# Kernel optimization log

Hardware: AMD Instinct MI355X
Metric: run time of the kernel (lower is better)

## Reference

```python
import jax, jax.numpy as jnp
import numpy as np

H = 8          # num_heads in nn.MultiheadAttention
TOP_K = 3
LN_EPS = 1e-5


def _layer_norm(x, gamma, beta):
    mu = x.mean(axis=-1, keepdims=True)
    var = ((x - mu) ** 2).mean(axis=-1, keepdims=True)
    return (x - mu) * jax.lax.rsqrt(var + LN_EPS) * gamma + beta


def setup_inputs() -> dict:
    key = jax.random.key(0)
    ks = jax.random.split(key, 12)
    B, T, D, N = 4, 4096, 1024, 64
    s = 0.02
    return {
        "current_frame": jax.random.normal(ks[0], (B, T, D), jnp.float32),
        "entity_memory": jax.random.normal(ks[1], (B, N, D), jnp.float32),
        "in_proj_w": jax.random.normal(ks[2], (3 * D, D), jnp.float32) * s,
        "in_proj_b": jax.random.normal(ks[3], (3 * D,), jnp.float32) * s,
        "out_proj_w": jax.random.normal(ks[4], (D, D), jnp.float32) * s,
        "out_proj_b": jax.random.normal(ks[5], (D,), jnp.float32) * s,
        "ln_gamma": jnp.ones((3, D), jnp.float32),
        "ln_beta": jnp.zeros((3, D), jnp.float32),
        "w1": jax.random.normal(ks[6], (3, 2 * D, D), jnp.float32) * s,
        "b1": jax.random.normal(ks[7], (3, 2 * D), jnp.float32) * s,
        "w2": jax.random.normal(ks[8], (3, D, 2 * D), jnp.float32) * s,
        "b2": jax.random.normal(ks[9], (3, D), jnp.float32) * s,
        "gate_w": jax.random.normal(ks[10], (D, 2 * D), jnp.float32) * s,
        "gate_b": jax.random.normal(ks[11], (D,), jnp.float32) * s,
    }


def reference(current_frame, entity_memory, in_proj_w, in_proj_b,
              out_proj_w, out_proj_b, ln_gamma, ln_beta, w1, b1, w2, b2,
              gate_w, gate_b):
    B, T, D = current_frame.shape
    N = entity_memory.shape[1]
    hd = D // H

    # --- nn.MultiheadAttention(q=frame, k=v=entity_memory), batch_first ---
    wq, wk, wv = in_proj_w[:D], in_proj_w[D:2 * D], in_proj_w[2 * D:]
    bq, bk, bv = in_proj_b[:D], in_proj_b[D:2 * D], in_proj_b[2 * D:]
    q = (current_frame @ wq.T + bq).reshape(B, T, H, hd).transpose(0, 2, 1, 3)
    k = (entity_memory @ wk.T + bk).reshape(B, N, H, hd).transpose(0, 2, 1, 3)
    v = (entity_memory @ wv.T + bv).reshape(B, N, H, hd).transpose(0, 2, 1, 3)
    scores = jnp.einsum('bhtd,bhnd->bhtn', q, k) / jnp.sqrt(jnp.float32(hd))
    attn = jax.nn.softmax(scores, axis=-1)                     # [B,H,T,N]
    ctx = jnp.einsum('bhtn,bhnd->bhtd', attn, v)
    ctx = ctx.transpose(0, 2, 1, 3).reshape(B, T, D)
    attended = ctx @ out_proj_w.T + out_proj_b
    attn_weights = attn.mean(axis=1)                           # avg over heads [B,T,N]

    # --- residual consistency MLP stack ---
    x = current_frame + attended
    for i in range(ln_gamma.shape[0]):
        h = _layer_norm(x, ln_gamma[i], ln_beta[i])
        h = jax.nn.gelu(h @ w1[i].T + b1[i], approximate=False)
        x = x + h @ w2[i].T + b2[i]

    # --- gated EMA entity-memory update ---
    frame_summary = current_frame.mean(axis=1, keepdims=True)   # [B,1,D]
    mem_summary = entity_memory.mean(axis=1, keepdims=True)     # [B,1,D]
    gate = jax.nn.sigmoid(
        jnp.concatenate([frame_summary, mem_summary], axis=-1) @ gate_w.T + gate_b)
    new_mem = gate * frame_summary + (1.0 - gate) * mem_summary  # [B,1,D]

    top_k = min(TOP_K, N)
    topk_idx = jax.lax.top_k(attn_weights.mean(axis=1), top_k)[1]  # [B,k]
    bidx = jnp.arange(B)[:, None]
    old = entity_memory[bidx, topk_idx]                          # [B,k,D]
    entity_memory = entity_memory.at[bidx, topk_idx].set(0.7 * old + 0.3 * new_mem)

    return x, entity_memory
```

## Files before the change

kernel.cpp:

```cpp
#include <hip/hip_runtime.h>
#include <hip/hip_bf16.h>
#include <cmath>

#define B_  4
#define T_  4096
#define D_  1024
#define N_  64
#define H_  8
#define HD_ 128
#define BT_ (B_*T_)
#define D2_ 2048

typedef __attribute__((ext_vector_type(8))) short bfrag8;
typedef __attribute__((ext_vector_type(4))) float f32x4;

__device__ __forceinline__ void gload_lds16(const void* g, void* l) {
    __builtin_amdgcn_global_load_lds(
        (const __attribute__((address_space(1))) unsigned int*)g,
        (__attribute__((address_space(3))) unsigned int*)l,
        16, 0, 0);
}

template<bool GELU, bool RES, bool OUTBF16>
__global__ __launch_bounds__(512, 2) void gemm_bf16_kernel(
    const __hip_bfloat16* __restrict__ A, const __hip_bfloat16* __restrict__ Wt,
    const float* __restrict__ bias, const float* __restrict__ res,
    void* __restrict__ Cout, int M, int N, int K)
{
    __shared__ short As[2 * 256 * 64];
    __shared__ short Bs[2 * 256 * 64];

    const int tid = threadIdx.x;
    const int lane = tid & 63;
    const int wid = tid >> 6;
    const int wr = wid >> 2;
    const int wc = wid & 3;

    const int nwg = gridDim.x * gridDim.y;
    int lin = blockIdx.y * gridDim.x + blockIdx.x;
    if ((nwg & 7) == 0) lin = (lin & 7) * (nwg >> 3) + (lin >> 3);
    const int by = lin / gridDim.x;
    const int bx = lin - by * gridDim.x;
    const int m0 = by * 256;
    const int n0 = bx * 256;

    const short* Ag = (const short*)A;
    const short* Bg = (const short*)Wt;

    const int frow = lane & 15;
    const int fk8  = lane >> 4;

    f32x4 acc[8][4] = {};

    const int nt = K >> 6;

    auto STAGE = [&](int t) {
        const int kb = t << 6;
        short* Ab = &As[(t & 1) * 16384];
        short* Bb = &Bs[(t & 1) * 16384];
#pragma unroll
        for (int s = 0; s < 4; ++s) {
            const int L = s * 512 + tid;
            const int row = L >> 3, p = L & 7;
            const int g8 = ((p ^ (row & 7)) << 3);
            gload_lds16(Ag + (size_t)(m0 + row) * K + kb + g8, &Ab[L * 8]);
            gload_lds16(Bg + (size_t)(n0 + row) * K + kb + g8, &Bb[L * 8]);
        }
    };

    STAGE(0);
    asm volatile("s_waitcnt vmcnt(0)" ::: "memory");
    __syncthreads();

    for (int t = 0; t < nt; ++t) {
        if (t + 1 < nt) STAGE(t + 1);
        const short* Ab = &As[(t & 1) * 16384];
        const short* Bb = &Bs[(t & 1) * 16384];
        for (int kk = 0; kk < 2; ++kk) {
            bfrag8 a[8], b[4];
#pragma unroll
            for (int i = 0; i < 8; ++i) {
                const int row = wr * 128 + i * 16 + frow;
                a[i] = *(const bfrag8*)&Ab[row * 64 + (((kk * 4 + fk8) ^ (row & 7)) << 3)];
            }
#pragma unroll
            for (int j = 0; j < 4; ++j) {
                const int row = wc * 64 + j * 16 + frow;
                b[j] = *(const bfrag8*)&Bb[row * 64 + (((kk * 4 + fk8) ^ (row & 7)) << 3)];
            }
#pragma unroll
            for (int i = 0; i < 8; ++i)
#pragma unroll
                for (int j = 0; j < 4; ++j)
                    acc[i][j] = __builtin_amdgcn_mfma_f32_16x16x32_bf16(a[i], b[j], acc[i][j], 0, 0, 0);
        }
        asm volatile("s_waitcnt vmcnt(0)" ::: "memory");
        __syncthreads();
    }

    float bias4[4];
#pragma unroll
    for (int j = 0; j < 4; ++j)
        bias4[j] = bias[n0 + wc * 64 + j * 16 + (lane & 15)];
#pragma unroll
    for (int i = 0; i < 8; ++i) {
        const int rbase = m0 + wr * 128 + i * 16 + (lane >> 4) * 4;
#pragma unroll
        for (int r = 0; r < 4; ++r) {
            const size_t rowoff = (size_t)(rbase + r) * N;
#pragma unroll
            for (int j = 0; j < 4; ++j) {
                const int col = n0 + wc * 64 + j * 16 + (lane & 15);
                float v = acc[i][j][r] + bias4[j];
                if (GELU) v = 0.5f * v * (1.0f + erff(v * 0.70710678118654752f));
                if (RES)  v += res[rowoff + col];
                if (OUTBF16) ((__hip_bfloat16*)Cout)[rowoff + col] = __float2bfloat16(v);
                else         ((float*)Cout)[rowoff + col] = v;
            }
        }
    }
}

__global__ __launch_bounds__(256) void cvt_kernel(
    const float* __restrict__ in, __hip_bfloat16* __restrict__ out, int n)
{
    const int i = (blockIdx.x * 256 + threadIdx.x) * 8;
    if (i >= n) return;
    const float4 v0 = *(const float4*)&in[i];
    const float4 v1 = *(const float4*)&in[i + 4];
    __hip_bfloat16 o[8];
    o[0] = __float2bfloat16(v0.x); o[1] = __float2bfloat16(v0.y);
    o[2] = __float2bfloat16(v0.z); o[3] = __float2bfloat16(v0.w);
    o[4] = __float2bfloat16(v1.x); o[5] = __float2bfloat16(v1.y);
    o[6] = __float2bfloat16(v1.z); o[7] = __float2bfloat16(v1.w);
    *(uint4*)&out[i] = *(uint4*)o;
}

__global__ __launch_bounds__(256) void ln_fused_kernel(
    const float* __restrict__ x, const float* __restrict__ g,
    const float* __restrict__ be, __hip_bfloat16* __restrict__ out)
{
    const int m = blockIdx.x;
    const int c = threadIdx.x * 4;
    const float4 v = *(const float4*)&x[(size_t)m * D_ + c];
    float s = v.x + v.y + v.z + v.w;
    float ss = v.x * v.x + v.y * v.y + v.z * v.z + v.w * v.w;
#pragma unroll
    for (int off = 32; off; off >>= 1) {
        s += __shfl_xor(s, off);
        ss += __shfl_xor(ss, off);
    }
    __shared__ float bs[4], bss[4];
    const int wave = threadIdx.x >> 6;
    if ((threadIdx.x & 63) == 0) { bs[wave] = s; bss[wave] = ss; }
    __syncthreads();
    const float S = bs[0] + bs[1] + bs[2] + bs[3];
    const float SS = bss[0] + bss[1] + bss[2] + bss[3];
    const float mean = S * (1.0f / D_);
    const float rstd = rsqrtf(SS * (1.0f / D_) - mean * mean + 1e-5f);
    const float4 gg = *(const float4*)&g[c];
    const float4 bb = *(const float4*)&be[c];
    __hip_bfloat16 o[4];
    o[0] = __float2bfloat16((v.x - mean) * rstd * gg.x + bb.x);
    o[1] = __float2bfloat16((v.y - mean) * rstd * gg.y + bb.y);
    o[2] = __float2bfloat16((v.z - mean) * rstd * gg.z + bb.z);
    o[3] = __float2bfloat16((v.w - mean) * rstd * gg.w + bb.w);
    *(uint2*)&out[(size_t)m * D_ + c] = *(uint2*)o;
}

__global__ __launch_bounds__(256) void vtrans_kernel(
    const __hip_bfloat16* __restrict__ vbb, __hip_bfloat16* __restrict__ vtb)
{
    const int bh = blockIdx.x;
    const int b = bh >> 3, h = bh & 7;
    for (int ii = threadIdx.x; ii < HD_ * N_; ii += 256) {
        const int d = ii >> 6, n = ii & 63;
        vtb[(size_t)bh * (HD_ * N_) + ii] =
            vbb[(size_t)(b * N_ + n) * D_ + h * HD_ + d];
    }
}

__global__ __launch_bounds__(256) void attn_mfma_kernel(
    const __hip_bfloat16* __restrict__ qb, const __hip_bfloat16* __restrict__ kbb,
    const __hip_bfloat16* __restrict__ vtb, __hip_bfloat16* __restrict__ ctxb,
    float* __restrict__ S)
{
    const int bh = blockIdx.y;
    const int b = bh >> 3, hh = bh & 7;
    const int t0 = blockIdx.x * 128;

    __shared__ short Ql[128 * 128];
    __shared__ short Kl[64 * 128];
    __shared__ short Vtl[128 * 64];
    __shared__ __hip_bfloat16 Pl[128 * 64];

    const int tid = threadIdx.x;
    const int lane = tid & 63;
    const int wid = tid >> 6;

    const short* qg = (const short*)qb;
    for (int s = wid; s < 32; s += 4) {
        const int row = 4 * s + (lane >> 4);
        const int col8 = (lane & 15) ^ (row & 7);
        gload_lds16(qg + ((size_t)(b * T_ + t0 + row)) * D_ + hh * HD_ + col8 * 8,
                    &Ql[s * 512 + lane * 8]);
    }
    const short* kg = (const short*)kbb;
    for (int s = wid; s < 16; s += 4) {
        const int row = 4 * s + (lane >> 4);
        const int col8 = (lane & 15) ^ (row & 7);
        gload_lds16(kg + ((size_t)(b * N_ + row)) * D_ + hh * HD_ + col8 * 8,
                    &Kl[s * 512 + lane * 8]);
    }
    const short* vg = (const short*)vtb + (size_t)bh * (HD_ * N_);
    for (int s = wid; s < 16; s += 4) {
        const int row = 8 * s + (lane >> 3);
        const int col8 = (lane & 7) ^ (row & 7);
        gload_lds16(vg + row * 64 + col8 * 8, &Vtl[s * 512 + lane * 8]);
    }
    __syncthreads();

    const int frow = lane & 15;
    const int fk8  = lane >> 4;

    f32x4 acc[2][4] = {};
#pragma unroll
    for (int ks = 0; ks < 4; ++ks) {
        bfrag8 a[2], bf[4];
#pragma unroll
        for (int i = 0; i < 2; ++i) {
            const int row = wid * 32 + i * 16 + frow;
            const int col8 = (ks * 4 + fk8) ^ (row & 7);
            a[i] = *(const bfrag8*)&Ql[row * 128 + col8 * 8];
        }
#pragma unroll
        for (int j = 0; j < 4; ++j) {
            const int row = j * 16 + frow;
            const int col8 = (ks * 4 + fk8) ^ (row & 7);
            bf[j] = *(const bfrag8*)&Kl[row * 128 + col8 * 8];
        }
#pragma unroll
        for (int i = 0; i < 2; ++i)
#pragma unroll
            for (int j = 0; j < 4; ++j)
                acc[i][j] = __builtin_amdgcn_mfma_f32_16x16x32_bf16(a[i], bf[j], acc[i][j], 0, 0, 0);
    }

    const float scale = 0.088388347648318441f;
    float accS[4] = {0.f, 0.f, 0.f, 0.f};
#pragma unroll
    for (int i = 0; i < 2; ++i) {
#pragma unroll
        for (int r = 0; r < 4; ++r) {
            float sv[4];
            float m = -INFINITY;
#pragma unroll
            for (int j = 0; j < 4; ++j) { sv[j] = acc[i][j][r] * scale; m = fmaxf(m, sv[j]); }
#pragma unroll
            for (int off = 1; off < 16; off <<= 1) m = fmaxf(m, __shfl_xor(m, off));
            float sum = 0.f;
#pragma unroll
            for (int j = 0; j < 4; ++j) { sv[j] = __expf(sv[j] - m); sum += sv[j]; }
#pragma unroll
            for (int off = 1; off < 16; off <<= 1) sum += __shfl_xor(sum, off);
            const float inv = 1.0f / sum;
            const int row = wid * 32 + i * 16 + (lane >> 4) * 4 + r;
#pragma unroll
            for (int j = 0; j < 4; ++j) {
                const float pn = sv[j] * inv;
                accS[j] += pn;
                const int col = j * 16 + (lane & 15);
                Pl[row * 64 + (((col >> 3) ^ (row & 7)) << 3) + (col & 7)] = __float2bfloat16(pn);
            }
        }
    }
#pragma unroll
    for (int j = 0; j < 4; ++j) {
        float v = accS[j];
        v += __shfl_xor(v, 16);
        v += __shfl_xor(v, 32);
        if (lane < 16)
            atomicAdd(&S[b * N_ + j * 16 + lane], v * (1.0f / (H_ * (float)T_)));
    }
    __syncthreads();

    f32x4 acc2[2][8] = {};
#pragma unroll
    for (int ks = 0; ks < 2; ++ks) {
        bfrag8 pa[2];
#pragma unroll
        for (int i = 0; i < 2; ++i) {
            const int row = wid * 32 + i * 16 + frow;
            const int col8 = (ks * 4 + fk8) ^ (row & 7);
            pa[i] = *(const bfrag8*)&Pl[row * 64 + col8 * 8];
        }
#pragma unroll
        for (int j = 0; j < 8; ++j) {
            const int row = j * 16 + frow;
            const int col8 = (ks * 4 + fk8) ^ (row & 7);
            const bfrag8 vv = *(const bfrag8*)&Vtl[row * 64 + col8 * 8];
#pragma unroll
            for (int i = 0; i < 2; ++i)
                acc2[i][j] = __builtin_amdgcn_mfma_f32_16x16x32_bf16(pa[i], vv, acc2[i][j], 0, 0, 0);
        }
    }

    short* Cl = Ql;
#pragma unroll
    for (int i = 0; i < 2; ++i)
#pragma unroll
        for (int r = 0; r < 4; ++r) {
            const int row = wid * 32 + i * 16 + (lane >> 4) * 4 + r;
#pragma unroll
            for (int j = 0; j < 8; ++j) {
                __hip_bfloat16 hv = __float2bfloat16(acc2[i][j][r]);
                Cl[row * 128 + j * 16 + (lane & 15)] = *(short*)&hv;
            }
        }
    __syncthreads();
    short* cg = (short*)ctxb;
#pragma unroll
    for (int s = 0; s < 8; ++s) {
        const int c = s * 256 + tid;
        const int row = c >> 4;
        const int slot = c & 15;
        *(uint4*)&cg[((size_t)(b * T_ + t0 + row)) * D_ + hh * HD_ + slot * 8] =
            *(const uint4*)&Cl[row * 128 + slot * 8];
    }
}

__global__ __launch_bounds__(256) void frame_summary_kernel(
    const float* __restrict__ cf, float* __restrict__ fs)
{
    const int b = blockIdx.x;
    const int d = blockIdx.y * 256 + threadIdx.x;
    const int t0 = blockIdx.z * 512;
    float s = 0.0f;
    for (int t = t0; t < t0 + 512; ++t)
        s += cf[((size_t)(b * T_ + t)) * D_ + d];
    atomicAdd(&fs[b * D_ + d], s * (1.0f / (float)T_));
}

__global__ __launch_bounds__(256) void mem_summary_kernel(
    const float* __restrict__ em, float* __restrict__ ms)
{
    const int b = blockIdx.x;
    const int d = blockIdx.y * 256 + threadIdx.x;
    float s = 0.0f;
#pragma unroll 4
    for (int n = 0; n < N_; ++n)
        s += em[((size_t)(b * N_ + n)) * D_ + d];
    ms[b * D_ + d] = s * (1.0f / (float)N_);
}

__global__ __launch_bounds__(256) void gate_kernel(
    const float* __restrict__ fs, const float* __restrict__ ms,
    const float* __restrict__ gw, const float* __restrict__ gb,
    float* __restrict__ nm)
{
    const int b = blockIdx.x;
    const int d = blockIdx.y * 256 + threadIdx.x;
    const float* wrow = gw + (size_t)d * D2_;
    const float* f = fs + b * D_;
    const float* mm = ms + b * D_;
    float g = gb[d];
    for (int j = 0; j < D_; ++j) g += f[j] * wrow[j];
    for (int j = 0; j < D_; ++j) g += mm[j] * wrow[D_ + j];
    const float sig = 1.0f / (1.0f + __expf(-g));
    nm[b * D_ + d] = sig * f[d] + (1.0f - sig) * mm[d];
}

__global__ __launch_bounds__(256) void topk_update_kernel(
    const float* __restrict__ S, const float* __restrict__ em,
    const float* __restrict__ nm, float* __restrict__ emo)
{
    const int b = blockIdx.x;
    __shared__ int topi[3];
    const int tid = threadIdx.x;
    if (tid < 64) {
        float sv = S[b * N_ + tid];
#pragma unroll
        for (int k = 0; k < 3; ++k) {
            float v = sv;
            int idx = tid;
#pragma unroll
            for (int off = 32; off; off >>= 1) {
                const float ov = __shfl_xor(v, off);
                const int oi = __shfl_xor(idx, off);
                if (ov > v || (ov == v && oi < idx)) { v = ov; idx = oi; }
            }
            if (tid == 0) topi[k] = idx;
            if (tid == idx) sv = -INFINITY;
        }
    }
    __syncthreads();
    const int i0 = topi[0], i1 = topi[1], i2 = topi[2];
    const float4* emb = (const float4*)(em + (size_t)b * N_ * D_);
    const float4* nmb = (const float4*)(nm + (size_t)b * D_);
    float4* outb = (float4*)(emo + (size_t)b * N_ * D_);
    for (int idx = tid; idx < N_ * D_ / 4; idx += 256) {
        const int n = idx >> 8;
        const int d4 = idx & 255;
        float4 v = emb[idx];
        if (n == i0 || n == i1 || n == i2) {
            const float4 nv = nmb[d4];
            v.x = 0.7f * v.x + 0.3f * nv.x;
            v.y = 0.7f * v.y + 0.3f * nv.y;
            v.z = 0.7f * v.z + 0.3f * nv.z;
            v.w = 0.7f * v.w + 0.3f * nv.w;
        }
        outb[idx] = v;
    }
}

extern "C" void kernel_launch(void* const* d_in, const int* in_sizes, int n_in,
                              void* d_out, int out_size, void* d_ws, size_t ws_size,
                              hipStream_t stream)
{
    const float* cf  = (const float*)d_in[0];
    const float* em  = (const float*)d_in[1];
    const float* ipw = (const float*)d_in[2];
    const float* ipb = (const float*)d_in[3];
    const float* opw = (const float*)d_in[4];
    const float* opb = (const float*)d_in[5];
    const float* lng = (const float*)d_in[6];
    const float* lnb = (const float*)d_in[7];
    const float* w1  = (const float*)d_in[8];
    const float* b1  = (const float*)d_in[9];
    const float* w2  = (const float*)d_in[10];
    const float* b2  = (const float*)d_in[11];
    const float* gw  = (const float*)d_in[12];
    const float* gb  = (const float*)d_in[13];

    float* x   = (float*)d_out;
    float* emo = x + (size_t)BT_ * D_;

    char* w = (char*)d_ws;
    __hip_bfloat16* h    = (__hip_bfloat16*)w;
    __hip_bfloat16* qbuf = (__hip_bfloat16*)w;
    w += 67108864;
    __hip_bfloat16* actb = (__hip_bfloat16*)w; w += 33554432;
    __hip_bfloat16* ipwb = (__hip_bfloat16*)w; w += 6291456;
    __hip_bfloat16* opwb = (__hip_bfloat16*)w; w += 2097152;
    __hip_bfloat16* w1b  = (__hip_bfloat16*)w; w += 12582912;
    __hip_bfloat16* w2b  = (__hip_bfloat16*)w; w += 12582912;
    __hip_bfloat16* emb  = (__hip_bfloat16*)w; w += 524288;
    __hip_bfloat16* kbb  = (__hip_bfloat16*)w; w += 524288;
    __hip_bfloat16* vbb  = (__hip_bfloat16*)w; w += 524288;
    __hip_bfloat16* vtb  = (__hip_bfloat16*)w; w += 524288;
    float* S  = (float*)w; w += 1024;
    float* fs = (float*)w; w += 16384;
    float* ms = (float*)w; w += 16384;
    float* nm = (float*)w; w += 16384;

    hipMemsetAsync(S, 0, (256 + 4096) * sizeof(float), stream);

    const dim3 blk(256);
    const dim3 blk512(512);

    cvt_kernel<<<8192, blk, 0, stream>>>(cf, actb, BT_ * D_);
    cvt_kernel<<<128,  blk, 0, stream>>>(em, emb, B_ * N_ * D_);
    cvt_kernel<<<1536, blk, 0, stream>>>(ipw, ipwb, 3 * D_ * D_);
    cvt_kernel<<<512,  blk, 0, stream>>>(opw, opwb, D_ * D_);
    cvt_kernel<<<3072, blk, 0, stream>>>(w1, w1b, 3 * D2_ * D_);
    cvt_kernel<<<3072, blk, 0, stream>>>(w2, w2b, 3 * D_ * D2_);

    gemm_bf16_kernel<false, false, true><<<dim3(4, 64), blk512, 0, stream>>>(
        actb, ipwb, ipb, nullptr, qbuf, BT_, D_, D_);
    gemm_bf16_kernel<false, false, true><<<dim3(4, 1), blk512, 0, stream>>>(
        emb, ipwb + D_ * D_, ipb + D_, nullptr, kbb, B_ * N_, D_, D_);
    gemm_bf16_kernel<false, false, true><<<dim3(4, 1), blk512, 0, stream>>>(
        emb, ipwb + 2 * D_ * D_, ipb + 2 * D_, nullptr, vbb, B_ * N_, D_, D_);
    vtrans_kernel<<<B_ * H_, blk, 0, stream>>>(vbb, vtb);

    attn_mfma_kernel<<<dim3(T_ / 128, B_ * H_), blk, 0, stream>>>(
        qbuf, kbb, vtb, actb, S);

    gemm_bf16_kernel<false, true, false><<<dim3(4, 64), blk512, 0, stream>>>(
        actb, opwb, opb, cf, x, BT_, D_, D_);

    for (int i = 0; i < 3; ++i) {
        ln_fused_kernel<<<BT_, blk, 0, stream>>>(
            x, lng + i * D_, lnb + i * D_, actb);
        gemm_bf16_kernel<true, false, true><<<dim3(8, 64), blk512, 0, stream>>>(
            actb, w1b + (size_t)i * D2_ * D_, b1 + i * D2_, nullptr, h,
            BT_, D2_, D_);
        gemm_bf16_kernel<false, true, false><<<dim3(4, 64), blk512, 0, stream>>>(
            h, w2b + (size_t)i * D_ * D2_, b2 + i * D_, x, x,
            BT_, D_, D2_);
    }

    frame_summary_kernel<<<dim3(B_, 4, 8), blk, 0, stream>>>(cf, fs);
    mem_summary_kernel<<<dim3(B_, 4), blk, 0, stream>>>(em, ms);
    gate_kernel<<<dim3(B_, 4), blk, 0, stream>>>(fs, ms, gw, gb, nm);
    topk_update_kernel<<<B_, blk, 0, stream>>>(S, em, nm, emo);
}
```

Measured before the change: 1.166 ms.

## Split GEMM K-loop into half-tile stages interleaved with MFMA and barriers

Measured after the change: 1.139 ms. 2.3% less time.

```diff
diff --git a/kernel.cpp b/kernel.cpp
--- a/kernel.cpp
+++ b/kernel.cpp
@@ -21,6 +21,11 @@
         16, 0, 0);
 }
 
+#define S_BARRIER()    __builtin_amdgcn_s_barrier()
+#define WAIT_LGKM0()   { asm volatile("s_waitcnt lgkmcnt(0)" ::: "memory"); \
+                         __builtin_amdgcn_sched_barrier(0); }
+#define WAIT_VM(n)     asm volatile("s_waitcnt vmcnt(" #n ")" ::: "memory")
+
 template<bool GELU, bool RES, bool OUTBF16>
 __global__ __launch_bounds__(512, 2) void gemm_bf16_kernel(
     const __hip_bfloat16* __restrict__ A, const __hip_bfloat16* __restrict__ Wt,
@@ -44,73 +49,122 @@
     const int m0 = by * 256;
     const int n0 = bx * 256;
 
-    const short* Ag = (const short*)A;
-    const short* Bg = (const short*)Wt;
+    const short* Ag = (const short*)A + (size_t)m0 * K;
+    const short* Bg = (const short*)Wt + (size_t)n0 * K;
 
     const int frow = lane & 15;
     const int fk8  = lane >> 4;
 
+    auto STAGE_A = [&](int t, int h) {
+        const int kb = t << 6;
+        short* Lb = &As[(t & 1) * 16384 + h * 8192];
+#pragma unroll
+        for (int s = 0; s < 2; ++s) {
+            const int L = s * 512 + tid;
+            const int row = h * 128 + (L >> 3), p = L & 7;
+            gload_lds16(Ag + (size_t)row * K + kb + ((p ^ (row & 7)) << 3), &Lb[L * 8]);
+        }
+    };
+    auto STAGE_B = [&](int t, int h) {
+        const int kb = t << 6;
+        short* Lb = &Bs[(t & 1) * 16384 + h * 8192];
+#pragma unroll
+        for (int s = 0; s < 2; ++s) {
+            const int L = s * 512 + tid;
+            const int row = h * 128 + (L >> 3), p = L & 7;
+            gload_lds16(Bg + (size_t)row * K + kb + ((p ^ (row & 7)) << 3), &Lb[L * 8]);
+        }
+    };
+
+    auto LDA = [&](int t, int i, int kk) -> bfrag8 {
+        const int row = wr * 64 + (i & 3) * 16 + (i >> 2) * 128 + frow;
+        return *(const bfrag8*)&As[(t & 1) * 16384 + row * 64 +
+                                   (((kk * 4 + fk8) ^ (row & 7)) << 3)];
+    };
+    auto LDB = [&](int t, int j, int kk) -> bfrag8 {
+        const int row = wc * 32 + (j & 1) * 16 + (j >> 1) * 128 + frow;
+        return *(const bfrag8*)&Bs[(t & 1) * 16384 + row * 64 +
+                                   (((kk * 4 + fk8) ^ (row & 7)) << 3)];
+    };
+
     f32x4 acc[8][4] = {};
+    bfrag8 aF[4][2], bF[4][2];
 
     const int nt = K >> 6;
 
-    auto STAGE = [&](int t) {
-        const int kb = t << 6;
-        short* Ab = &As[(t & 1) * 16384];
-        short* Bb = &Bs[(t & 1) * 16384];
-#pragma unroll
-        for (int s = 0; s < 4; ++s) {
-            const int L = s * 512 + tid;
-            const int row = L >> 3, p = L & 7;
-            const int g8 = ((p ^ (row & 7)) << 3);
-            gload_lds16(Ag + (size_t)(m0 + row) * K + kb + g8, &Ab[L * 8]);
-            gload_lds16(Bg + (size_t)(n0 + row) * K + kb + g8, &Bb[L * 8]);
-        }
-    };
-
-    STAGE(0);
-    asm volatile("s_waitcnt vmcnt(0)" ::: "memory");
-    __syncthreads();
+    STAGE_A(0, 0); STAGE_B(0, 0); STAGE_B(0, 1); STAGE_A(0, 1);
+    WAIT_VM(4);
+    S_BARRIER();
 
     for (int t = 0; t < nt; ++t) {
-        if (t + 1 < nt) STAGE(t + 1);
-        const short* Ab = &As[(t & 1) * 16384];
-        const short* Bb = &Bs[(t & 1) * 16384];
-        for (int kk = 0; kk < 2; ++kk) {
-            bfrag8 a[8], b[4];
-#pragma unroll
-            for (int i = 0; i < 8; ++i) {
-                const int row = wr * 128 + i * 16 + frow;
-                a[i] = *(const bfrag8*)&Ab[row * 64 + (((kk * 4 + fk8) ^ (row & 7)) << 3)];
-            }
+        const bool nx = (t + 1 < nt);
+#pragma unroll
+        for (int ii = 0; ii < 4; ++ii) { aF[ii][0] = LDA(t, ii, 0); aF[ii][1] = LDA(t, ii, 1); }
+#pragma unroll
+        for (int j = 0; j < 2; ++j)    { bF[j][0] = LDB(t, j, 0);  bF[j][1] = LDB(t, j, 1); }
+        if (nx) STAGE_A(t + 1, 0);
+        S_BARRIER();
+        WAIT_LGKM0();
+        __builtin_amdgcn_s_setprio(1);
+#pragma unroll
+        for (int ii = 0; ii < 4; ++ii)
+#pragma unroll
+            for (int j = 0; j < 2; ++j) {
+                acc[ii][j] = __builtin_amdgcn_mfma_f32_16x16x32_bf16(aF[ii][0], bF[j][0], acc[ii][j], 0, 0, 0);
+                acc[ii][j] = __builtin_amdgcn_mfma_f32_16x16x32_bf16(aF[ii][1], bF[j][1], acc[ii][j], 0, 0, 0);
+            }
+        __builtin_amdgcn_s_setprio(0);
+        if (nx) { WAIT_VM(4); } else { WAIT_VM(2); }
+        S_BARRIER();
+
+#pragma unroll
+        for (int j = 2; j < 4; ++j)    { bF[j][0] = LDB(t, j, 0);  bF[j][1] = LDB(t, j, 1); }
+        if (nx) STAGE_B(t + 1, 0);
+        S_BARRIER();
+        WAIT_LGKM0();
+        __builtin_amdgcn_s_setprio(1);
+#pragma unroll
+        for (int ii = 0; ii < 4; ++ii)
+#pragma unroll
+            for (int j = 2; j < 4; ++j) {
+                acc[ii][j] = __builtin_amdgcn_mfma_f32_16x16x32_bf16(aF[ii][0], bF[j][0], acc[ii][j], 0, 0, 0);
+                acc[ii][j] = __builtin_amdgcn_mfma_f32_16x16x32_bf16(aF[ii][1], bF[j][1], acc[ii][j], 0, 0, 0);
+            }
+        __builtin_amdgcn_s_setprio(0);
+        if (nx) { WAIT_VM(4); } else { WAIT_VM(0); }
+        S_BARRIER();
+
+#pragma unroll
+        for (int ii = 0; ii < 4; ++ii) { aF[ii][0] = LDA(t, 4 + ii, 0); aF[ii][1] = LDA(t, 4 + ii, 1); }
+        if (nx) { STAGE_B(t + 1, 1); STAGE_A(t + 1, 1); }
+        S_BARRIER();
+        WAIT_LGKM0();
+        __builtin_amdgcn_s_setprio(1);
+#pragma unroll
+        for (int ii = 0; ii < 4; ++ii)
 #pragma unroll
             for (int j = 0; j < 4; ++j) {
-                const int row = wc * 64 + j * 16 + frow;
-                b[j] = *(const bfrag8*)&Bb[row * 64 + (((kk * 4 + fk8) ^ (row & 7)) << 3)];
-            }
-#pragma unroll
-            for (int i = 0; i < 8; ++i)
-#pragma unroll
-                for (int j = 0; j < 4; ++j)
-                    acc[i][j] = __builtin_amdgcn_mfma_f32_16x16x32_bf16(a[i], b[j], acc[i][j], 0, 0, 0);
-        }
-        asm volatile("s_waitcnt vmcnt(0)" ::: "memory");
-        __syncthreads();
+                acc[4 + ii][j] = __builtin_amdgcn_mfma_f32_16x16x32_bf16(aF[ii][0], bF[j][0], acc[4 + ii][j], 0, 0, 0);
+                acc[4 + ii][j] = __builtin_amdgcn_mfma_f32_16x16x32_bf16(aF[ii][1], bF[j][1], acc[4 + ii][j], 0, 0, 0);
+            }
+        __builtin_amdgcn_s_setprio(0);
+        if (nx) { WAIT_VM(4); }
+        S_BARRIER();
     }
 
     float bias4[4];
 #pragma unroll
     for (int j = 0; j < 4; ++j)
-        bias4[j] = bias[n0 + wc * 64 + j * 16 + (lane & 15)];
+        bias4[j] = bias[n0 + wc * 32 + (j & 1) * 16 + (j >> 1) * 128 + (lane & 15)];
 #pragma unroll
     for (int i = 0; i < 8; ++i) {
-        const int rbase = m0 + wr * 128 + i * 16 + (lane >> 4) * 4;
+        const int rbase = m0 + wr * 64 + (i & 3) * 16 + (i >> 2) * 128 + (lane >> 4) * 4;
 #pragma unroll
         for (int r = 0; r < 4; ++r) {
             const size_t rowoff = (size_t)(rbase + r) * N;
 #pragma unroll
             for (int j = 0; j < 4; ++j) {
-                const int col = n0 + wc * 64 + j * 16 + (lane & 15);
+                const int col = n0 + wc * 32 + (j & 1) * 16 + (j >> 1) * 128 + (lane & 15);
                 float v = acc[i][j][r] + bias4[j];
                 if (GELU) v = 0.5f * v * (1.0f + erff(v * 0.70710678118654752f));
                 if (RES)  v += res[rowoff + col];
```
